# Optimization experiments

Hardware: AMD Instinct MI355X
Metric: run time of the kernel (lower is better)

## Reference

```python
import jax, jax.numpy as jnp
import numpy as np

N = 4096
IN_DIM = 1433
HID = 64
OUT_DIM = 7
LAM_HAT = 0.9
LAM = 1.0 / LAM_HAT - 1.0          # skip-connection weight lambda
SCAD_A = 3.7
K_STEPS = 10
AVG_DEG = 32


def setup_inputs() -> dict:
    key = jax.random.key(0)
    k_a, k_x, k_w1, k_w2 = jax.random.split(key, 4)
    # symmetric binary adjacency, avg degree ~AVG_DEG, zero diagonal
    U = jax.random.uniform(k_a, (N, N), dtype=jnp.float32)
    p = AVG_DEG / N
    A = (jnp.minimum(U, U.T) < p).astype(jnp.float32)
    A = A * (1.0 - jnp.eye(N, dtype=jnp.float32))
    X = jax.random.normal(k_x, (N, IN_DIM), dtype=jnp.float32)
    w1 = jax.random.normal(k_w1, (IN_DIM, HID), dtype=jnp.float32) * (1.0 / np.sqrt(IN_DIM))
    b1 = jnp.zeros((HID,), dtype=jnp.float32)
    w2 = jax.random.normal(k_w2, (HID, OUT_DIM), dtype=jnp.float32) * (1.0 / np.sqrt(HID))
    b2 = jnp.zeros((OUT_DIM,), dtype=jnp.float32)
    log_gamma_0 = jnp.asarray(np.log(3.0), dtype=jnp.float32)          # gamma_0_init = 3.0
    raw_decay = jnp.asarray(np.log(0.85 / 0.15), dtype=jnp.float32)    # logit(0.85)
    return {"A": A, "X": X, "w1": w1, "b1": b1, "w2": w2, "b2": b2,
            "log_gamma_0": log_gamma_0, "raw_decay": raw_decay}


def _scad_weight(y, lam_k):
    """SCAD IRLS edge weight: 1 for y<=lam, linear roll-off to 0 at y=a*lam."""
    y_safe = jnp.maximum(y, 1e-12)  # avoid 0/0 in unselected branch
    w_mid = (SCAD_A * lam_k - y) / ((SCAD_A - 1.0) * y_safe)
    return jnp.where(y <= lam_k, 1.0,
                     jnp.where(y <= SCAD_A * lam_k, w_mid, 0.0))


def reference(A, X, w1, b1, w2, b2, log_gamma_0, raw_decay):
    # 1. MLP (eval mode: dropout = identity): X -> F0 in class space [N, C]
    F0 = jax.nn.relu(X @ w1 + b1) @ w2 + b2

    n = A.shape[0]
    eye = jnp.eye(n, dtype=A.dtype)
    A = A + eye                                   # add_loops
    D = A.sum(-1)                                 # [N]
    D_sq = jnp.sqrt(D)[:, None]                   # [N,1]
    d_is = 1.0 / jnp.sqrt(D)
    A_tilde = A * d_is[:, None] * d_is[None, :]   # sym_norm

    g0 = jnp.exp(log_gamma_0)
    r = jax.nn.sigmoid(raw_decay)

    F = F0
    for k in range(K_STEPS):
        gamma_k = g0 * (r ** k)
        lam_k = gamma_k / SCAD_A
        # pairwise squared Euclidean of degree-normalized features (detached)
        Fn = jax.lax.stop_gradient(F / D_sq)      # [N,C]
        sq = jnp.sum(Fn * Fn, axis=-1)
        Z = jnp.maximum(sq[:, None] + sq[None, :] - 2.0 * (Fn @ Fn.T), 0.0)
        y = jnp.sqrt(Z)                           # [N,N]
        W = _scad_weight(y, lam_k)
        W = W * (1.0 - eye)                       # zero diagonal
        W = jnp.where(jnp.isnan(W), 1.0, W)       # NaN guard (as in torch code)
        Q_hat = ((W * A).sum(-1) / D + LAM)[:, None]   # [N,1]
        F = (W * A_tilde) @ F / Q_hat + LAM * F0 / Q_hat
    return F


if __name__ == "__main__":
    out = reference(**setup_inputs())
    print(out.shape, out.dtype)
```

## Files before the change

kernel.cpp:

```cpp
#include <hip/hip_runtime.h>
#include <math.h>

#define N_NODES 4096
#define IN_DIM  1433
#define HID     64
#define OUT_DIM 7
#define FPAD    8
#define CAP     128
#define BR      64
#define KT      32
#define LPN     16

static constexpr float LAMBDA = (float)(1.0 / 0.9 - 1.0);
static constexpr float SCADA  = 3.7f;

__global__ __launch_bounds__(256) void build_adj(const float* __restrict__ A,
    int* __restrict__ nbr, int* __restrict__ cnt, float* __restrict__ deg,
    float* __restrict__ rsd, float* __restrict__ lamt,
    const float* __restrict__ lg0p, const float* __restrict__ rdp) {
  int i = blockIdx.x;
  if (i == 0 && threadIdx.x == 0) {
    float r_ = 1.0f / (1.0f + expf(-rdp[0]));
    float g  = expf(lg0p[0]) * (1.0f / SCADA);
    #pragma unroll
    for (int k = 0; k < 10; ++k) { lamt[k] = g; g *= r_; }
  }
  __shared__ int c;
  if (threadIdx.x == 0) c = 0;
  __syncthreads();
  const float4* row = (const float4*)(A + (size_t)i * N_NODES);
  for (int q = threadIdx.x; q < N_NODES / 4; q += 256) {
    float4 v = row[q];
    int j0 = q * 4;
    if (v.x != 0.0f) { int s = atomicAdd(&c, 1); if (s < CAP) nbr[(size_t)i * CAP + s] = j0; }
    if (v.y != 0.0f) { int s = atomicAdd(&c, 1); if (s < CAP) nbr[(size_t)i * CAP + s] = j0 + 1; }
    if (v.z != 0.0f) { int s = atomicAdd(&c, 1); if (s < CAP) nbr[(size_t)i * CAP + s] = j0 + 2; }
    if (v.w != 0.0f) { int s = atomicAdd(&c, 1); if (s < CAP) nbr[(size_t)i * CAP + s] = j0 + 3; }
  }
  __syncthreads();
  if (threadIdx.x == 0) {
    int cc = c; if (cc > CAP) cc = CAP;
    cnt[i] = cc;
    float d = (float)c + 1.0f;
    deg[i] = d;
    rsd[i] = 1.0f / sqrtf(d);
  }
}

__global__ __launch_bounds__(128) void pack_edges(const int* __restrict__ nbr,
    const int* __restrict__ cnt, const float* __restrict__ rsd,
    int2* __restrict__ ej) {
  int i = blockIdx.x;
  int s = threadIdx.x;
  if (s < cnt[i]) {
    int j = nbr[(size_t)i * CAP + s];
    ej[(size_t)i * CAP + s] = make_int2(j, __float_as_int(rsd[j]));
  }
}

__global__ __launch_bounds__(256) void gemm1(const float* __restrict__ X,
    const float* __restrict__ w1, float* __restrict__ P, int ksplit) {
  __shared__ __align__(16) float Xs[KT][BR + 4];
  __shared__ __align__(16) float Ws[KT][HID];
  const int t  = threadIdx.x;
  const int r0 = blockIdx.x * BR;
  const int ks = blockIdx.y;
  const int kbeg = (IN_DIM * ks) / ksplit;
  const int kend = (IN_DIM * (ks + 1)) / ksplit;
  const int rg = t >> 4;
  const int cg = t & 15;

  float acc[4][4];
  #pragma unroll
  for (int r = 0; r < 4; ++r)
    #pragma unroll
    for (int c = 0; c < 4; ++c) acc[r][c] = 0.0f;

  for (int k0 = kbeg; k0 < kend; k0 += KT) {
    #pragma unroll
    for (int j = 0; j < (BR * KT) / 256; ++j) {
      int e = t + 256 * j;
      int row = e >> 5;
      int kk  = e & (KT - 1);
      int k   = k0 + kk;
      float v = (k < kend) ? X[(size_t)(r0 + row) * IN_DIM + k] : 0.0f;
      Xs[kk][row] = v;
    }
    #pragma unroll
    for (int j = 0; j < (HID * KT) / 256; ++j) {
      int e = t + 256 * j;
      int kk  = e >> 6;
      int col = e & 63;
      int k   = k0 + kk;
      Ws[kk][col] = (k < kend) ? w1[(size_t)k * HID + col] : 0.0f;
    }
    __syncthreads();
    #pragma unroll
    for (int kk = 0; kk < KT; ++kk) {
      const float4 xv = *(const float4*)&Xs[kk][rg * 4];
      const float4 wv = *(const float4*)&Ws[kk][cg * 4];
      float xr[4] = {xv.x, xv.y, xv.z, xv.w};
      float wc[4] = {wv.x, wv.y, wv.z, wv.w};
      #pragma unroll
      for (int r = 0; r < 4; ++r)
        #pragma unroll
        for (int c = 0; c < 4; ++c) acc[r][c] += xr[r] * wc[c];
    }
    __syncthreads();
  }
  float* Pp = P + (size_t)ks * N_NODES * HID;
  #pragma unroll
  for (int r = 0; r < 4; ++r) {
    int row = r0 + rg * 4 + r;
    float4 v = make_float4(acc[r][0], acc[r][1], acc[r][2], acc[r][3]);
    *(float4*)&Pp[(size_t)row * HID + cg * 4] = v;
  }
}

__global__ __launch_bounds__(256) void reduce_h(const float* __restrict__ P,
    float* __restrict__ H, int ksplit) {
  int idx4 = blockIdx.x * 256 + threadIdx.x;
  const float4* P4 = (const float4*)P;
  float4 s = P4[idx4];
  for (int ks = 1; ks < ksplit; ++ks) {
    float4 v = P4[(size_t)ks * (N_NODES * HID / 4) + idx4];
    s.x += v.x; s.y += v.y; s.z += v.z; s.w += v.w;
  }
  ((float4*)H)[idx4] = s;
}

__global__ __launch_bounds__(256) void mlp_out(const float* __restrict__ H,
    const float* __restrict__ b1, const float* __restrict__ w2,
    const float* __restrict__ b2, float* __restrict__ F0, float* __restrict__ Fcur) {
  int t = blockIdx.x * blockDim.x + threadIdx.x;
  if (t >= N_NODES * FPAD) return;
  int row = t >> 3, c = t & 7;
  if (c == 7) { F0[t] = 0.0f; Fcur[t] = 0.0f; return; }
  float acc = b2[c];
  const float* h = H + (size_t)row * HID;
  #pragma unroll
  for (int k = 0; k < HID; ++k) {
    float hv = fmaxf(h[k] + b1[k], 0.0f);
    acc += hv * w2[k * OUT_DIM + c];
  }
  F0[t] = acc;
  Fcur[t] = acc;
}

__global__ __launch_bounds__(256) void rung_step(const float* __restrict__ Fin,
    const float* __restrict__ F0, float* __restrict__ Fout,
    const int2* __restrict__ ej, const int* __restrict__ cnt,
    const float* __restrict__ deg, const float* __restrict__ rsd,
    const float* __restrict__ lamt, int kstep, int last) {
  const int lane = threadIdx.x & (LPN - 1);
  const int i = (blockIdx.x * 256 + threadIdx.x) / LPN;

  const float lam = lamt[kstep];
  const float rsi = rsd[i];
  const float Di  = deg[i];
  const int   ci  = cnt[i];

  float Fni[FPAD];
  {
    const float4* fp = (const float4*)(Fin + (size_t)i * FPAD);
    float4 a0 = fp[0], a1 = fp[1];
    Fni[0] = a0.x * rsi; Fni[1] = a0.y * rsi; Fni[2] = a0.z * rsi; Fni[3] = a0.w * rsi;
    Fni[4] = a1.x * rsi; Fni[5] = a1.y * rsi; Fni[6] = a1.z * rsi; Fni[7] = a1.w * rsi;
  }
  float s = 0.0f;
  float acc[FPAD] = {0, 0, 0, 0, 0, 0, 0, 0};
  const int2* ep = ej + (size_t)i * CAP;
  for (int l = lane; l < ci; l += LPN) {
    int2 e = ep[l];
    int   j   = e.x;
    float rsj = __int_as_float(e.y);
    const float4* fp = (const float4*)(Fin + (size_t)j * FPAD);
    float4 b0 = fp[0], b1v = fp[1];
    float fj[FPAD] = {b0.x, b0.y, b0.z, b0.w, b1v.x, b1v.y, b1v.z, b1v.w};
    float d2 = 0.0f;
    #pragma unroll
    for (int c = 0; c < FPAD; ++c) {
      float df = Fni[c] - fj[c] * rsj;
      d2 += df * df;
    }
    float y = sqrtf(d2);
    float w;
    if (y <= lam)              w = 1.0f;
    else if (y <= SCADA * lam) w = (SCADA * lam - y) / ((SCADA - 1.0f) * fmaxf(y, 1e-12f));
    else                       w = 0.0f;
    if (w != w) w = 1.0f;
    s += w;
    float wr = w * rsi * rsj;
    #pragma unroll
    for (int c = 0; c < FPAD; ++c) acc[c] += wr * fj[c];
  }
  #pragma unroll
  for (int off = LPN / 2; off > 0; off >>= 1) {
    s += __shfl_xor(s, off, LPN);
    #pragma unroll
    for (int c = 0; c < FPAD; ++c) acc[c] += __shfl_xor(acc[c], off, LPN);
  }
  if (lane == 0) {
    float Q = s / Di + LAMBDA;
    float inv = 1.0f / Q;
    if (last) {
      #pragma unroll
      for (int c = 0; c < OUT_DIM; ++c)
        Fout[(size_t)i * OUT_DIM + c] = (acc[c] + LAMBDA * F0[(size_t)i * FPAD + c]) * inv;
    } else {
      float o[FPAD];
      #pragma unroll
      for (int c = 0; c < FPAD; ++c)
        o[c] = (acc[c] + LAMBDA * F0[(size_t)i * FPAD + c]) * inv;
      float4* op = (float4*)(Fout + (size_t)i * FPAD);
      op[0] = make_float4(o[0], o[1], o[2], o[3]);
      op[1] = make_float4(o[4], o[5], o[6], o[7]);
    }
  }
}

extern "C" void kernel_launch(void* const* d_in, const int* in_sizes, int n_in,
                              void* d_out, int out_size, void* d_ws, size_t ws_size,
                              hipStream_t stream) {
  const float* A   = (const float*)d_in[0];
  const float* X   = (const float*)d_in[1];
  const float* w1  = (const float*)d_in[2];
  const float* b1  = (const float*)d_in[3];
  const float* w2  = (const float*)d_in[4];
  const float* b2  = (const float*)d_in[5];
  const float* lg0 = (const float*)d_in[6];
  const float* rd  = (const float*)d_in[7];
  float* out = (float*)d_out;

  const size_t fixed = (size_t)N_NODES * CAP * sizeof(int)
                     + (size_t)N_NODES * sizeof(int)
                     + (size_t)N_NODES * sizeof(float) * 2
                     + (size_t)N_NODES * CAP * sizeof(int2)
                     + (size_t)N_NODES * HID * sizeof(float)
                     + (size_t)N_NODES * FPAD * sizeof(float) * 3
                     + 64;
  const size_t pbuf = (size_t)N_NODES * HID * sizeof(float);
  int ksplit = (ws_size >= fixed + 16 * pbuf) ? 16 : 8;

  char* w = (char*)d_ws;
  int*   nbr = (int*)w;   w += (size_t)N_NODES * CAP * sizeof(int);
  int*   cnt = (int*)w;   w += (size_t)N_NODES * sizeof(int);
  float* deg = (float*)w; w += (size_t)N_NODES * sizeof(float);
  float* rsd = (float*)w; w += (size_t)N_NODES * sizeof(float);
  int2*  ej  = (int2*)w;  w += (size_t)N_NODES * CAP * sizeof(int2);
  float* P   = (float*)w; w += (size_t)ksplit * N_NODES * HID * sizeof(float);
  float* H   = (float*)w; w += (size_t)N_NODES * HID * sizeof(float);
  float* F0  = (float*)w; w += (size_t)N_NODES * FPAD * sizeof(float);
  float* FA  = (float*)w; w += (size_t)N_NODES * FPAD * sizeof(float);
  float* FB  = (float*)w; w += (size_t)N_NODES * FPAD * sizeof(float);
  float* lamt = (float*)w;

  build_adj<<<N_NODES, 256, 0, stream>>>(A, nbr, cnt, deg, rsd, lamt, lg0, rd);
  pack_edges<<<N_NODES, 128, 0, stream>>>(nbr, cnt, rsd, ej);
  gemm1<<<dim3(N_NODES / BR, ksplit), 256, 0, stream>>>(X, w1, P, ksplit);
  reduce_h<<<(N_NODES * HID / 4) / 256, 256, 0, stream>>>(P, H, ksplit);
  mlp_out<<<(N_NODES * FPAD) / 256, 256, 0, stream>>>(H, b1, w2, b2, F0, FA);

  float* cur = FA;
  float* nxt = FB;
  for (int k = 0; k < 10; ++k) {
    int last = (k == 9);
    float* dst = last ? out : nxt;
    rung_step<<<(N_NODES * LPN) / 256, 256, 0, stream>>>(cur, F0, dst, ej, cnt,
                                                         deg, rsd, lamt, k, last);
    float* tmp = cur; cur = nxt; nxt = tmp;
  }
}
```

Before: 209.6 us.

## Fuse adjacency build with split-K GEMM and merge reduce with MLP output

Puts adjacency extraction and the split-K first-layer GEMM into one launch with heterogeneous block roles, so the memory-bound A scan and the compute-bound GEMM can run concurrently. The split-K reduction and the second MLP layer are fused into one wave-per-row kernel that uses shuffle reductions, which drops the intermediate H buffer. The packed edge array is also removed, so rung_step now gathers rsd[j] indirectly, adding an extra dependent load in every iteration. The net effect is fewer launches and less intermediate traffic.

Measured after the change: 206.7 us. About the same (-1.4%).

```diff
diff --git a/kernel.cpp b/kernel.cpp
--- a/kernel.cpp
+++ b/kernel.cpp
@@ -14,61 +14,56 @@
 static constexpr float LAMBDA = (float)(1.0 / 0.9 - 1.0);
 static constexpr float SCADA  = 3.7f;
 
-__global__ __launch_bounds__(256) void build_adj(const float* __restrict__ A,
+__global__ __launch_bounds__(256) void front(const float* __restrict__ A,
+    const float* __restrict__ X, const float* __restrict__ w1,
     int* __restrict__ nbr, int* __restrict__ cnt, float* __restrict__ deg,
-    float* __restrict__ rsd, float* __restrict__ lamt,
-    const float* __restrict__ lg0p, const float* __restrict__ rdp) {
-  int i = blockIdx.x;
-  if (i == 0 && threadIdx.x == 0) {
-    float r_ = 1.0f / (1.0f + expf(-rdp[0]));
-    float g  = expf(lg0p[0]) * (1.0f / SCADA);
-    #pragma unroll
-    for (int k = 0; k < 10; ++k) { lamt[k] = g; g *= r_; }
-  }
-  __shared__ int c;
-  if (threadIdx.x == 0) c = 0;
-  __syncthreads();
-  const float4* row = (const float4*)(A + (size_t)i * N_NODES);
-  for (int q = threadIdx.x; q < N_NODES / 4; q += 256) {
-    float4 v = row[q];
-    int j0 = q * 4;
-    if (v.x != 0.0f) { int s = atomicAdd(&c, 1); if (s < CAP) nbr[(size_t)i * CAP + s] = j0; }
-    if (v.y != 0.0f) { int s = atomicAdd(&c, 1); if (s < CAP) nbr[(size_t)i * CAP + s] = j0 + 1; }
-    if (v.z != 0.0f) { int s = atomicAdd(&c, 1); if (s < CAP) nbr[(size_t)i * CAP + s] = j0 + 2; }
-    if (v.w != 0.0f) { int s = atomicAdd(&c, 1); if (s < CAP) nbr[(size_t)i * CAP + s] = j0 + 3; }
-  }
-  __syncthreads();
-  if (threadIdx.x == 0) {
-    int cc = c; if (cc > CAP) cc = CAP;
-    cnt[i] = cc;
-    float d = (float)c + 1.0f;
-    deg[i] = d;
-    rsd[i] = 1.0f / sqrtf(d);
-  }
-}
-
-__global__ __launch_bounds__(128) void pack_edges(const int* __restrict__ nbr,
-    const int* __restrict__ cnt, const float* __restrict__ rsd,
-    int2* __restrict__ ej) {
-  int i = blockIdx.x;
-  int s = threadIdx.x;
-  if (s < cnt[i]) {
-    int j = nbr[(size_t)i * CAP + s];
-    ej[(size_t)i * CAP + s] = make_int2(j, __float_as_int(rsd[j]));
-  }
-}
-
-__global__ __launch_bounds__(256) void gemm1(const float* __restrict__ X,
-    const float* __restrict__ w1, float* __restrict__ P, int ksplit) {
-  __shared__ __align__(16) float Xs[KT][BR + 4];
-  __shared__ __align__(16) float Ws[KT][HID];
-  const int t  = threadIdx.x;
-  const int r0 = blockIdx.x * BR;
-  const int ks = blockIdx.y;
+    float* __restrict__ rsd, float* __restrict__ P, float* __restrict__ lamt,
+    const float* __restrict__ lg0p, const float* __restrict__ rdp, int ksplit) {
+  __shared__ __align__(16) float lds[KT * (BR + 4) + KT * HID];
+  const int b = blockIdx.x;
+  const int t = threadIdx.x;
+
+  if (b < N_NODES) {
+    const int i = b;
+    if (i == 0 && t == 0) {
+      float r_ = 1.0f / (1.0f + expf(-rdp[0]));
+      float g  = expf(lg0p[0]) * (1.0f / SCADA);
+      #pragma unroll
+      for (int k = 0; k < 10; ++k) { lamt[k] = g; g *= r_; }
+    }
+    int* cp = (int*)lds;
+    if (t == 0) *cp = 0;
+    __syncthreads();
+    const float4* row = (const float4*)(A + (size_t)i * N_NODES);
+    for (int q = t; q < N_NODES / 4; q += 256) {
+      float4 v = row[q];
+      int j0 = q * 4;
+      if (v.x != 0.0f) { int s = atomicAdd(cp, 1); if (s < CAP) nbr[(size_t)i * CAP + s] = j0; }
+      if (v.y != 0.0f) { int s = atomicAdd(cp, 1); if (s < CAP) nbr[(size_t)i * CAP + s] = j0 + 1; }
+      if (v.z != 0.0f) { int s = atomicAdd(cp, 1); if (s < CAP) nbr[(size_t)i * CAP + s] = j0 + 2; }
+      if (v.w != 0.0f) { int s = atomicAdd(cp, 1); if (s < CAP) nbr[(size_t)i * CAP + s] = j0 + 3; }
+    }
+    __syncthreads();
+    if (t == 0) {
+      int cc = *cp; if (cc > CAP) cc = CAP;
+      cnt[i] = cc;
+      float d = (float)(*cp) + 1.0f;
+      deg[i] = d;
+      rsd[i] = 1.0f / sqrtf(d);
+    }
+    return;
+  }
+
+  const int bb = b - N_NODES;
+  const int rb = bb & (N_NODES / BR - 1);
+  const int ks = bb >> 6;
+  const int r0 = rb * BR;
   const int kbeg = (IN_DIM * ks) / ksplit;
   const int kend = (IN_DIM * (ks + 1)) / ksplit;
   const int rg = t >> 4;
   const int cg = t & 15;
+  float* Xs = lds;
+  float* Ws = lds + KT * (BR + 4);
 
   float acc[4][4];
   #pragma unroll
@@ -84,7 +79,7 @@
       int kk  = e & (KT - 1);
       int k   = k0 + kk;
       float v = (k < kend) ? X[(size_t)(r0 + row) * IN_DIM + k] : 0.0f;
-      Xs[kk][row] = v;
+      Xs[kk * (BR + 4) + row] = v;
     }
     #pragma unroll
     for (int j = 0; j < (HID * KT) / 256; ++j) {
@@ -92,13 +87,13 @@
       int kk  = e >> 6;
       int col = e & 63;
       int k   = k0 + kk;
-      Ws[kk][col] = (k < kend) ? w1[(size_t)k * HID + col] : 0.0f;
+      Ws[kk * HID + col] = (k < kend) ? w1[(size_t)k * HID + col] : 0.0f;
     }
     __syncthreads();
     #pragma unroll
     for (int kk = 0; kk < KT; ++kk) {
-      const float4 xv = *(const float4*)&Xs[kk][rg * 4];
-      const float4 wv = *(const float4*)&Ws[kk][cg * 4];
+      const float4 xv = *(const float4*)&Xs[kk * (BR + 4) + rg * 4];
+      const float4 wv = *(const float4*)&Ws[kk * HID + cg * 4];
       float xr[4] = {xv.x, xv.y, xv.z, xv.w};
       float wc[4] = {wv.x, wv.y, wv.z, wv.w};
       #pragma unroll
@@ -117,39 +112,52 @@
   }
 }
 
-__global__ __launch_bounds__(256) void reduce_h(const float* __restrict__ P,
-    float* __restrict__ H, int ksplit) {
-  int idx4 = blockIdx.x * 256 + threadIdx.x;
-  const float4* P4 = (const float4*)P;
-  float4 s = P4[idx4];
-  for (int ks = 1; ks < ksplit; ++ks) {
-    float4 v = P4[(size_t)ks * (N_NODES * HID / 4) + idx4];
-    s.x += v.x; s.y += v.y; s.z += v.z; s.w += v.w;
-  }
-  ((float4*)H)[idx4] = s;
-}
-
-__global__ __launch_bounds__(256) void mlp_out(const float* __restrict__ H,
+__global__ __launch_bounds__(256) void reduce_mlp(const float* __restrict__ P,
     const float* __restrict__ b1, const float* __restrict__ w2,
-    const float* __restrict__ b2, float* __restrict__ F0, float* __restrict__ Fcur) {
-  int t = blockIdx.x * blockDim.x + threadIdx.x;
-  if (t >= N_NODES * FPAD) return;
-  int row = t >> 3, c = t & 7;
-  if (c == 7) { F0[t] = 0.0f; Fcur[t] = 0.0f; return; }
-  float acc = b2[c];
-  const float* h = H + (size_t)row * HID;
-  #pragma unroll
-  for (int k = 0; k < HID; ++k) {
-    float hv = fmaxf(h[k] + b1[k], 0.0f);
-    acc += hv * w2[k * OUT_DIM + c];
-  }
-  F0[t] = acc;
-  Fcur[t] = acc;
+    const float* __restrict__ b2, float* __restrict__ F0,
+    float* __restrict__ Fcur, int ksplit) {
+  const int wave = threadIdx.x >> 6;
+  const int lane = threadIdx.x & 63;
+  const int row  = blockIdx.x * 4 + wave;
+
+  float h = 0.0f;
+  const float* p = P + (size_t)row * HID + lane;
+  for (int ks = 0; ks < ksplit; ++ks)
+    h += p[(size_t)ks * N_NODES * HID];
+  float hv = fmaxf(h + b1[lane], 0.0f);
+
+  float a0 = hv * w2[lane * OUT_DIM + 0];
+  float a1 = hv * w2[lane * OUT_DIM + 1];
+  float a2 = hv * w2[lane * OUT_DIM + 2];
+  float a3 = hv * w2[lane * OUT_DIM + 3];
+  float a4 = hv * w2[lane * OUT_DIM + 4];
+  float a5 = hv * w2[lane * OUT_DIM + 5];
+  float a6 = hv * w2[lane * OUT_DIM + 6];
+  #pragma unroll
+  for (int off = 32; off > 0; off >>= 1) {
+    a0 += __shfl_xor(a0, off);
+    a1 += __shfl_xor(a1, off);
+    a2 += __shfl_xor(a2, off);
+    a3 += __shfl_xor(a3, off);
+    a4 += __shfl_xor(a4, off);
+    a5 += __shfl_xor(a5, off);
+    a6 += __shfl_xor(a6, off);
+  }
+  if (lane == 0) {
+    float o[FPAD] = {a0 + b2[0], a1 + b2[1], a2 + b2[2], a3 + b2[3],
+                     a4 + b2[4], a5 + b2[5], a6 + b2[6], 0.0f};
+    float4 v0 = make_float4(o[0], o[1], o[2], o[3]);
+    float4 v1 = make_float4(o[4], o[5], o[6], o[7]);
+    float4* f0p = (float4*)(F0  + (size_t)row * FPAD);
+    float4* fcp = (float4*)(Fcur + (size_t)row * FPAD);
+    f0p[0] = v0; f0p[1] = v1;
+    fcp[0] = v0; fcp[1] = v1;
+  }
 }
 
 __global__ __launch_bounds__(256) void rung_step(const float* __restrict__ Fin,
     const float* __restrict__ F0, float* __restrict__ Fout,
-    const int2* __restrict__ ej, const int* __restrict__ cnt,
+    const int* __restrict__ nbr, const int* __restrict__ cnt,
     const float* __restrict__ deg, const float* __restrict__ rsd,
     const float* __restrict__ lamt, int kstep, int last) {
   const int lane = threadIdx.x & (LPN - 1);
@@ -169,11 +177,10 @@
   }
   float s = 0.0f;
   float acc[FPAD] = {0, 0, 0, 0, 0, 0, 0, 0};
-  const int2* ep = ej + (size_t)i * CAP;
+  const int* nb = nbr + (size_t)i * CAP;
   for (int l = lane; l < ci; l += LPN) {
-    int2 e = ep[l];
-    int   j   = e.x;
-    float rsj = __int_as_float(e.y);
+    int j = nb[l];
+    float rsj = rsd[j];
     const float4* fp = (const float4*)(Fin + (size_t)j * FPAD);
     float4 b0 = fp[0], b1v = fp[1];
     float fj[FPAD] = {b0.x, b0.y, b0.z, b0.w, b1v.x, b1v.y, b1v.z, b1v.w};
@@ -235,8 +242,6 @@
   const size_t fixed = (size_t)N_NODES * CAP * sizeof(int)
                      + (size_t)N_NODES * sizeof(int)
                      + (size_t)N_NODES * sizeof(float) * 2
-                     + (size_t)N_NODES * CAP * sizeof(int2)
-                     + (size_t)N_NODES * HID * sizeof(float)
                      + (size_t)N_NODES * FPAD * sizeof(float) * 3
                      + 64;
   const size_t pbuf = (size_t)N_NODES * HID * sizeof(float);
@@ -247,26 +252,22 @@
   int*   cnt = (int*)w;   w += (size_t)N_NODES * sizeof(int);
   float* deg = (float*)w; w += (size_t)N_NODES * sizeof(float);
   float* rsd = (float*)w; w += (size_t)N_NODES * sizeof(float);
-  int2*  ej  = (int2*)w;  w += (size_t)N_NODES * CAP * sizeof(int2);
   float* P   = (float*)w; w += (size_t)ksplit * N_NODES * HID * sizeof(float);
-  float* H   = (float*)w; w += (size_t)N_NODES * HID * sizeof(float);
   float* F0  = (float*)w; w += (size_t)N_NODES * FPAD * sizeof(float);
   float* FA  = (float*)w; w += (size_t)N_NODES * FPAD * sizeof(float);
   float* FB  = (float*)w; w += (size_t)N_NODES * FPAD * sizeof(float);
   float* lamt = (float*)w;
 
-  build_adj<<<N_NODES, 256, 0, stream>>>(A, nbr, cnt, deg, rsd, lamt, lg0, rd);
-  pack_edges<<<N_NODES, 128, 0, stream>>>(nbr, cnt, rsd, ej);
-  gemm1<<<dim3(N_NODES / BR, ksplit), 256, 0, stream>>>(X, w1, P, ksplit);
-  reduce_h<<<(N_NODES * HID / 4) / 256, 256, 0, stream>>>(P, H, ksplit);
-  mlp_out<<<(N_NODES * FPAD) / 256, 256, 0, stream>>>(H, b1, w2, b2, F0, FA);
+  front<<<N_NODES + (N_NODES / BR) * ksplit, 256, 0, stream>>>(
+      A, X, w1, nbr, cnt, deg, rsd, P, lamt, lg0, rd, ksplit);
+  reduce_mlp<<<N_NODES / 4, 256, 0, stream>>>(P, b1, w2, b2, F0, FA, ksplit);
 
   float* cur = FA;
   float* nxt = FB;
   for (int k = 0; k < 10; ++k) {
     int last = (k == 9);
     float* dst = last ? out : nxt;
-    rung_step<<<(N_NODES * LPN) / 256, 256, 0, stream>>>(cur, F0, dst, ej, cnt,
+    rung_step<<<(N_NODES * LPN) / 256, 256, 0, stream>>>(cur, F0, dst, nbr, cnt,
                                                          deg, rsd, lamt, k, last);
     float* tmp = cur; cur = nxt; nxt = tmp;
   }
```
